# Kernel optimization log

Hardware: AMD Instinct MI355X
Metric: run time of the kernel (lower is better)

The kernel has to match this reference:

```python
import jax, jax.numpy as jnp
import numpy as np
from jax import lax

E = 5      # NUM_EXPERTS
K = 3      # top-k
DIN = 32 * 10 * 10  # 3200
DH = 128
NCLS = 10


def setup_inputs() -> dict:
    key = jax.random.key(0)
    ks = jax.random.split(key, 16)
    s = 0.02
    return {
        "x": jax.random.normal(ks[0], (8192, 1, 28, 28), dtype=jnp.float32),
        "conv1_w": jax.random.normal(ks[1], (16, 1, 5, 5), dtype=jnp.float32) * s,
        "conv1_b": jnp.zeros((16,), jnp.float32),
        "conv2_w": jax.random.normal(ks[2], (32, 16, 3, 3), dtype=jnp.float32) * s,
        "conv2_b": jnp.zeros((32,), jnp.float32),
        "Wg": jax.random.normal(ks[3], (DIN, E), dtype=jnp.float32) * s,
        "bg": jnp.zeros((E,), jnp.float32),
        "Wglu": jax.random.normal(ks[4], (DIN, E), dtype=jnp.float32) * s,
        "bglu": jnp.zeros((E,), jnp.float32),
        "W1e": jax.random.normal(ks[5], (E, DIN, DH), dtype=jnp.float32) * s,
        "b1e": jnp.zeros((E, DH), jnp.float32),
        "W2e": jax.random.normal(ks[6], (E, DH, DH), dtype=jnp.float32) * s,
        "b2e": jnp.zeros((E, DH), jnp.float32),
        "Ws": jax.random.normal(ks[7], (DH, NCLS), dtype=jnp.float32) * s,
        "bs": jnp.zeros((NCLS,), jnp.float32),
    }


def _conv(x, w, b):
    y = lax.conv_general_dilated(x, w, (1, 1), 'VALID',
                                 dimension_numbers=('NCHW', 'OIHW', 'NCHW'))
    return y + b[None, :, None, None]


def _maxpool2(x):
    return lax.reduce_window(x, -jnp.inf, lax.max, (1, 1, 2, 2), (1, 1, 2, 2), 'VALID')


def reference(x, conv1_w, conv1_b, conv2_w, conv2_b, Wg, bg, Wglu, bglu,
              W1e, b1e, W2e, b2e, Ws, bs):
    # conv feature extractor: [B,1,28,28] -> [B,3200]
    h = jax.nn.relu(_conv(x, conv1_w, conv1_b))          # [B,16,24,24]
    h = _maxpool2(h)                                     # [B,16,12,12]
    h = jax.nn.relu(_conv(h, conv2_w, conv2_b))          # [B,32,10,10]
    feat = h.reshape(h.shape[0], -1)                     # [B,3200]

    # GLU-gated router: logits * sigmoid(glu)
    h_act = feat @ Wg + bg                               # [B,E]
    h_glu_act = jax.nn.sigmoid(feat @ Wglu + bglu)       # [B,E]
    gate_logits = h_act * h_glu_act                      # [B,E]

    # top-K routing with softmax over selected logits
    top_v, top_i = lax.top_k(gate_logits, K)             # [B,K]
    top_w = jax.nn.softmax(top_v, axis=-1)               # [B,K]
    onehot = jax.nn.one_hot(top_i, E, dtype=feat.dtype)  # [B,K,E]
    weights = jnp.einsum('bk,bke->be', top_w, onehot)    # [B,E]

    # experts (dense compute of all E=5 experts, masked combine)
    e1 = jnp.tanh(jnp.einsum('bd,edh->beh', feat, W1e) + b1e[None])  # [B,E,128]
    e2 = jnp.tanh(jnp.einsum('beh,ehg->beg', e1, W2e) + b2e[None])   # [B,E,128]
    moe_out = jnp.einsum('beg,be->bg', e2, weights)      # [B,128]

    logits = moe_out @ Ws + bs                           # [B,10]
    return jax.nn.softmax(logits, axis=1)
```

## Files before the change

kernel.cpp:

```cpp
#include <hip/hip_runtime.h>
#include <stdint.h>

typedef unsigned short u16;
typedef __attribute__((ext_vector_type(8))) short bf16x8;
typedef __attribute__((ext_vector_type(4))) float f32x4;

#define MFMA16(a, b, c) __builtin_amdgcn_mfma_f32_16x16x32_bf16((a), (b), (c), 0, 0, 0)
#define GLD16(gp, lp) __builtin_amdgcn_global_load_lds( \
    (__attribute__((address_space(1))) void*)(gp), \
    (__attribute__((address_space(3))) void*)(lp), 16, 0, 0)

__device__ __forceinline__ u16 f2b(float f) {
  uint32_t u = __float_as_uint(f);
  u += 0x7FFFu + ((u >> 16) & 1u);
  return (u16)(u >> 16);
}
__device__ __forceinline__ float tanhfast(float x) {
  float e = __expf(2.f * x);
  return (e - 1.f) / (e + 1.f);
}


__global__ __launch_bounds__(256) void prep_misc_kernel(
    const float* __restrict__ c2w, const float* __restrict__ Wg,
    const float* __restrict__ Wglu, const float* __restrict__ W2e,
    u16* __restrict__ W2colF, u16* __restrict__ WcatT, u16* __restrict__ W2T) {
  int i = blockIdx.x * 256 + threadIdx.x;
  if (i < 5120) {
    int j = i & 7, l = (i >> 3) & 63, nt = (i >> 9) & 1, s = i >> 10;
    int k = s * 32 + ((l >> 4) & 3) * 8 + j;
    int n = (l & 15) + nt * 16;
    float v = 0.f;
    if (k < 144) {
      int kykx = k >> 4, ci = k & 15;
      int ky = kykx / 3, kx = kykx - ky * 3;
      v = c2w[((n * 16 + ci) * 3 + ky) * 3 + kx];
    }
    W2colF[i] = f2b(v);
  } else if (i < 56320) {
    int o = i - 5120;
    int s = o >> 9, rest = o & 511;
    int l = rest >> 3, j = rest & 7;
    int r = l & 15, c = (l >> 4) * 8 + j;
    int dref = c * 100 + s;
    float v = 0.f;
    if (r < 5) v = Wg[dref * 5 + r];
    else if (r < 10) v = Wglu[dref * 5 + (r - 5)];
    WcatT[o] = f2b(v);
  } else if (i < 138240) {
    int o = i - 56320;
    int e = o >> 14, rem = o & 16383;
    int g = rem >> 7, h = rem & 127;
    W2T[o] = f2b(W2e[(e * 128 + h) * 128 + g]);
  }
}

__global__ __launch_bounds__(256) void prep_w1t_kernel(
    const float* __restrict__ W1e, u16* __restrict__ W1T) {
  __shared__ u16 ts[64][128];
  int t = threadIdx.x;
  int e = blockIdx.x / 50, pt = blockIdx.x % 50;
  {
    int r64 = t >> 2;
    int ph = r64 >> 5, c = r64 & 31;
    int d = c * 100 + pt * 2 + ph;
    const float* src = W1e + ((size_t)e * 3200 + d) * 128 + (t & 3) * 32;
    u16* drow = &ts[r64][(t & 3) * 32];
#pragma unroll
    for (int u = 0; u < 8; u++) {
      float4 v = *(const float4*)(src + u * 4);
      drow[u * 4 + 0] = f2b(v.x); drow[u * 4 + 1] = f2b(v.y);
      drow[u * 4 + 2] = f2b(v.z); drow[u * 4 + 3] = f2b(v.w);
    }
  }
  __syncthreads();
#pragma unroll
  for (int k = 0; k < 4; k++) {
    int u = t + k * 256;
    int ph = u >> 9, nb = (u >> 6) & 7, l = u & 63;
    int lm = l & 15, lqf = l >> 4;
    u16 tmp[8];
#pragma unroll
    for (int j = 0; j < 8; j++)
      tmp[j] = ts[ph * 32 + lqf * 8 + j][nb * 16 + lm];
    *(uint4*)(W1T + (((size_t)((e * 100 + pt * 2 + ph) * 8 + nb)) << 9) + l * 8) =
        *(const uint4*)tmp;
  }
}

__global__ __launch_bounds__(192) void conv1_kernel(
    const float* __restrict__ x, const float* __restrict__ w1,
    const float* __restrict__ b1, u16* __restrict__ h1) {
  __shared__ float xs[784];
  __shared__ float wsh[400];
  __shared__ float bsh[16];
  int t = threadIdx.x, b = blockIdx.x;
  const float4* xg = (const float4*)(x + (size_t)b * 784);
  float4* xs4 = (float4*)xs;
  for (int i = t; i < 196; i += 192) xs4[i] = xg[i];
  for (int i = t; i < 400; i += 192) wsh[i] = w1[i];
  if (t < 16) bsh[t] = b1[t];
  __syncthreads();
  int oc = t & 15, q0 = t >> 4;
  float w[25];
#pragma unroll
  for (int k = 0; k < 25; k++) w[k] = wsh[oc * 25 + k];
  float bias = bsh[oc];
  u16* out = h1 + (size_t)b * 2304;
#pragma unroll
  for (int it = 0; it < 6; it++) {
    int q = q0 + 12 * it;
    int py = q / 6, px2 = q - py * 6;
    int y0 = 2 * py, x0 = 4 * px2;
    float win[6][8];
#pragma unroll
    for (int r = 0; r < 6; r++) {
      const float4* p = (const float4*)&xs[(y0 + r) * 28 + x0];
      float4 a = p[0], c = p[1];
      win[r][0] = a.x; win[r][1] = a.y; win[r][2] = a.z; win[r][3] = a.w;
      win[r][4] = c.x; win[r][5] = c.y; win[r][6] = c.z; win[r][7] = c.w;
    }
#pragma unroll
    for (int half = 0; half < 2; half++) {
      int dxb = 2 * half;
      float c00 = 0.f, c01 = 0.f, c10 = 0.f, c11 = 0.f;
#pragma unroll
      for (int ky = 0; ky < 5; ky++)
#pragma unroll
        for (int kx = 0; kx < 5; kx++) {
          float wv = w[ky * 5 + kx];
          c00 += wv * win[ky][dxb + kx];
          c01 += wv * win[ky][dxb + kx + 1];
          c10 += wv * win[ky + 1][dxb + kx];
          c11 += wv * win[ky + 1][dxb + kx + 1];
        }
      float m = fmaxf(fmaxf(c00, c01), fmaxf(c10, c11)) + bias;
      m = fmaxf(m, 0.f);
      int px = 2 * px2 + half;
      out[(py * 12 + px) * 16 + oc] = f2b(m);
    }
  }
}

__global__ __launch_bounds__(256) void conv2_kernel(
    const u16* __restrict__ h1, const u16* __restrict__ W2colF,
    const float* __restrict__ b2, u16* __restrict__ feat) {
  __shared__ u16 ct[4][16][32];
  int t = threadIdx.x;
  int w = t >> 6, l = t & 63;
  bf16x8 bfr[5][2];
#pragma unroll
  for (int s = 0; s < 5; s++)
#pragma unroll
    for (int nt = 0; nt < 2; nt++)
      bfr[s][nt] = *(const bf16x8*)(W2colF + ((size_t)(s * 2 + nt) * 64 + l) * 8);
  int lm = l & 15, lq = l >> 4, hi = l >> 5;
  int cib = (lq & 1) * 8;
  float bias0 = b2[lm], bias1 = b2[lm + 16];
  int g0 = blockIdx.x * 128 + w * 32;
#pragma unroll
  for (int sub = 0; sub < 2; sub++) {
    int g = g0 + sub * 16 + lm;
    uint32_t bimg = (uint32_t)(((uint64_t)(uint32_t)g * 1374389535ull) >> 37);
    int p = g - (int)bimg * 100;
    int y = (p * 205) >> 11;
    int xc = p - y * 10;
    const u16* base = h1 + (size_t)bimg * 2304;
    f32x4 acc0 = {0.f, 0.f, 0.f, 0.f}, acc1 = {0.f, 0.f, 0.f, 0.f};
#pragma unroll
    for (int s = 0; s < 5; s++) {
      int kk = 2 * s + hi;
      if (kk > 8) kk = 8;
      int ky = (kk * 11) >> 5;
      int kx = kk - ky * 3;
      int off = ((y + ky) * 12 + (xc + kx)) * 16 + cib;
      bf16x8 a = *(const bf16x8*)(base + off);
      acc0 = MFMA16(a, bfr[s][0], acc0);
      acc1 = MFMA16(a, bfr[s][1], acc1);
    }
#pragma unroll
    for (int rr = 0; rr < 4; rr++) {
      ct[w][lq * 4 + rr][lm]      = f2b(fmaxf(acc0[rr] + bias0, 0.f));
      ct[w][lq * 4 + rr][lm + 16] = f2b(fmaxf(acc1[rr] + bias1, 0.f));
    }
    int gg = g0 + sub * 16 + (l >> 2);
    uint32_t bi2 = (uint32_t)(((uint64_t)(uint32_t)gg * 1374389535ull) >> 37);
    int pp = gg - (int)bi2 * 100;
    int mt2 = (int)(bi2 >> 6), rb = (int)((bi2 >> 4) & 3), lmr = (int)(bi2 & 15);
    uint4 v = *(const uint4*)&ct[w][l >> 2][(l & 3) * 8];
    *(uint4*)(feat + (((size_t)(mt2 * 100 + pp) * 4 + rb) << 9) +
              ((l & 3) * 16 + lmr) * 8) = v;
  }
}

#define GEMM1_KLOOP(HASW, VMCSTR)                                              \
  {                                                                            \
    GLD16(pA, &lds[0][w * 512]);                                               \
    GLD16(pB1, &lds[0][2048 + w * 512]);                                       \
    GLD16(pB2, &lds[0][4096 + w * 512]);                                       \
    if (HASW) GLD16(pW, &lds[0][6144]);                                        \
    pA += 2048; pB1 += 4096; pB2 += 4096; pW += 512;                           \
    for (int s = 0; s < 100; s++) {                                            \
      int buf = s & 1;                                                         \
      if (s < 99) {                                                            \
        GLD16(pA, &lds[buf ^ 1][w * 512]);                                     \
        GLD16(pB1, &lds[buf ^ 1][2048 + w * 512]);                             \
        GLD16(pB2, &lds[buf ^ 1][4096 + w * 512]);                             \
        if (HASW) GLD16(pW, &lds[buf ^ 1][6144]);                              \
        pA += 2048; pB1 += 4096; pB2 += 4096; pW += 512;                       \
        asm volatile("s_waitcnt " VMCSTR ::: "memory");                        \
      } else {                                                                 \
        asm volatile("s_waitcnt vmcnt(0)" ::: "memory");                       \
      }                                                                        \
      asm volatile("s_barrier" ::: "memory");                                  \
      const u16* st = &lds[buf][0];                                            \
      bf16x8 af[2], bf[4];                                                     \
      _Pragma("unroll")                                                        \
      for (int i = 0; i < 2; i++)                                              \
        af[i] = *(const bf16x8*)(st + ((w & 1) * 2 + i) * 512 + l * 8);        \
      _Pragma("unroll")                                                        \
      for (int j = 0; j < 4; j++)                                              \
        bf[j] = *(const bf16x8*)(st + 2048 + ((w >> 1) * 4 + j) * 512 + l * 8);\
      _Pragma("unroll")                                                        \
      for (int i = 0; i < 2; i++)                                              \
        _Pragma("unroll")                                                      \
        for (int j = 0; j < 4; j++)                                            \
          acc[i][j] = MFMA16(af[i], bf[j], acc[i][j]);                         \
      if (HASW && w < 2) {                                                     \
        bf16x8 wf = *(const bf16x8*)(st + 6144 + l * 8);                       \
        racc[0] = MFMA16(af[0], wf, racc[0]);                                  \
        racc[1] = MFMA16(af[1], wf, racc[1]);                                  \
      }                                                                        \
      asm volatile("s_barrier" ::: "memory");                                  \
    }                                                                          \
  }

__global__ __launch_bounds__(256, 3) void gemm1_kernel(
    const u16* __restrict__ feat, const u16* __restrict__ W1T,
    const u16* __restrict__ WcatT, const float* __restrict__ b1e,
    const float* __restrict__ bg, const float* __restrict__ bglu,
    u16* __restrict__ e1b, float* __restrict__ rw) {
  __shared__ u16 lds[2][6656];
  int t = threadIdx.x, w = t >> 6, l = t & 63;
  int mt = blockIdx.x & 127;
  int e = blockIdx.x >> 7;
  size_t m0 = (size_t)mt * 64;
  int lm = l & 15, lq = l >> 4;
  int m_off = (w & 1) * 32, n_off = (w >> 1) * 64;

  const u16* pA = feat + (size_t)mt * 204800 + w * 512 + l * 8;
  const u16* pB1 = W1T + (size_t)e * 409600 + w * 512 + l * 8;
  const u16* pB2 = pB1 + 2048;
  const u16* pW = WcatT + l * 8;

  f32x4 acc[2][4] = {};
  f32x4 racc[2] = {};

  if (e == 0) GEMM1_KLOOP(true, "vmcnt(4)")
  else        GEMM1_KLOOP(false, "vmcnt(3)")

  float b1v[4];
#pragma unroll
  for (int j = 0; j < 4; j++) b1v[j] = b1e[e * 128 + n_off + 16 * j + lm];
  u16* E1t = &lds[0][0];
#pragma unroll
  for (int i = 0; i < 2; i++)
#pragma unroll
    for (int j = 0; j < 4; j++)
#pragma unroll
      for (int rr = 0; rr < 4; rr++) {
        int row = m_off + 16 * i + lq * 4 + rr;
        int col = n_off + 16 * j + lm;
        E1t[row * 128 + col] = f2b(tanhfast(acc[i][j][rr] + b1v[j]));
      }
  if (e == 0 && w < 2) {
    float* RACC = (float*)((char*)lds + 20480);
#pragma unroll
    for (int i = 0; i < 2; i++)
#pragma unroll
      for (int rr = 0; rr < 4; rr++)
        RACC[(m_off + 16 * i + lq * 4 + rr) * 16 + lm] = racc[i][rr];
  }
  __syncthreads();
#pragma unroll
  for (int k2 = 0; k2 < 4; k2++) {
    int u = t + k2 * 256;
    int row = u >> 4, sc = u & 15;
    uint4 v = *(const uint4*)(E1t + row * 128 + sc * 8);
    *(uint4*)(e1b + (m0 + row) * 640 + e * 128 + sc * 8) = v;
  }
  if (e == 0 && t < 64) {
    const float* RACC = (const float*)((char*)lds + 20480);
    float gt[5];
#pragma unroll
    for (int ee = 0; ee < 5; ee++) {
      float va = RACC[t * 16 + ee] + bg[ee];
      float vb = RACC[t * 16 + 5 + ee] + bglu[ee];
      gt[ee] = va * (1.f / (1.f + __expf(-vb)));
    }
    float w3[3]; int i3[3];
    unsigned used = 0;
#pragma unroll
    for (int k = 0; k < 3; k++) {
      float best = -1e30f; int bi = 0;
#pragma unroll
      for (int ee = 0; ee < 5; ee++)
        if (!((used >> ee) & 1u) && gt[ee] > best) { best = gt[ee]; bi = ee; }
      used |= 1u << bi; w3[k] = best; i3[k] = bi;
    }
    float s1 = __expf(w3[1] - w3[0]), s2 = __expf(w3[2] - w3[0]);
    float inv = 1.f / (1.f + s1 + s2);
    float o[5] = {0.f, 0.f, 0.f, 0.f, 0.f};
    o[i3[0]] = inv; o[i3[1]] = s1 * inv; o[i3[2]] = s2 * inv;
#pragma unroll
    for (int ee = 0; ee < 5; ee++) rw[(m0 + t) * 5 + ee] = o[ee];
  }
}

__global__ __launch_bounds__(256) void gemm2_head_kernel(
    const u16* __restrict__ e1b, const u16* __restrict__ W2T,
    const float* __restrict__ b2e, const float* __restrict__ rw,
    const float* __restrict__ Ws, const float* __restrict__ bs,
    float* __restrict__ out) {
  __shared__ u16 E1s[32][648];
  __shared__ float wssh[1280];
  __shared__ float rws[160];
  int t = threadIdx.x;
  int r0 = blockIdx.x * 32;
  {
    int row = t >> 3;
    const u16* src = e1b + (size_t)(r0 + row) * 640 + (t & 7) * 8;
    u16* drow = &E1s[row][(t & 7) * 8];
#pragma unroll
    for (int k = 0; k < 10; k++)
      *(uint4*)(drow + k * 64) = *(const uint4*)(src + k * 64);
  }
  if (t < 160) rws[t] = rw[r0 * 5 + t];
  for (int i = t; i < 1280; i += 256) wssh[i] = Ws[i];
  __syncthreads();

  int w = t >> 6, l = t & 63, lm = l & 15, lq = l >> 4;
  int mh = w & 1, nh = w >> 1;
  f32x4 moeacc[4] = {};
#pragma unroll
  for (int e = 0; e < 5; e++) {
    f32x4 acc[4] = {};
    const u16* w2e = W2T + e * 16384;
#pragma unroll
    for (int kk = 0; kk < 4; kk++) {
      bf16x8 a = *(const bf16x8*)&E1s[mh * 16 + lm][e * 128 + kk * 32 + lq * 8];
#pragma unroll
      for (int j = 0; j < 4; j++) {
        bf16x8 b = *(const bf16x8*)(w2e + (nh * 64 + 16 * j + lm) * 128 + kk * 32 + lq * 8);
        acc[j] = MFMA16(a, b, acc[j]);
      }
    }
#pragma unroll
    for (int j = 0; j < 4; j++) {
      float b2v = b2e[e * 128 + nh * 64 + 16 * j + lm];
#pragma unroll
      for (int rr = 0; rr < 4; rr++) {
        float v = tanhfast(acc[j][rr] + b2v);
        moeacc[j][rr] += rws[(mh * 16 + lq * 4 + rr) * 5 + e] * v;
      }
    }
  }
  __syncthreads();
  float* moes = (float*)&E1s[0][0];
#pragma unroll
  for (int j = 0; j < 4; j++)
#pragma unroll
    for (int rr = 0; rr < 4; rr++)
      moes[(mh * 16 + lq * 4 + rr) * 132 + nh * 64 + 16 * j + lm] = moeacc[j][rr];
  __syncthreads();
  float* parts = moes + 32 * 132;
  if (t < 128) {
    int row = t >> 2, qc = t & 3;
    float pl[10] = {};
    for (int cc = qc * 32; cc < qc * 32 + 32; cc++) {
      float mv = moes[row * 132 + cc];
#pragma unroll
      for (int cls = 0; cls < 10; cls++) pl[cls] += mv * wssh[cc * 10 + cls];
    }
#pragma unroll
    for (int cls = 0; cls < 10; cls++) parts[(row * 4 + qc) * 10 + cls] = pl[cls];
  }
  __syncthreads();
  if (t < 32) {
    float lg[10];
    float mx = -1e30f;
#pragma unroll
    for (int cls = 0; cls < 10; cls++) {
      lg[cls] = parts[(t * 4) * 10 + cls] + parts[(t * 4 + 1) * 10 + cls] +
                parts[(t * 4 + 2) * 10 + cls] + parts[(t * 4 + 3) * 10 + cls] + bs[cls];
      mx = fmaxf(mx, lg[cls]);
    }
    float sum = 0.f;
#pragma unroll
    for (int cls = 0; cls < 10; cls++) { lg[cls] = __expf(lg[cls] - mx); sum += lg[cls]; }
    float inv = 1.f / sum;
    float* orow = out + (size_t)(r0 + t) * 10;
#pragma unroll
    for (int cls = 0; cls < 10; cls++) orow[cls] = lg[cls] * inv;
  }
}

extern "C" void kernel_launch(void* const* d_in, const int* in_sizes, int n_in,
                              void* d_out, int out_size, void* d_ws, size_t ws_size,
                              hipStream_t stream) {
  const float* x    = (const float*)d_in[0];
  const float* c1w  = (const float*)d_in[1];
  const float* c1b  = (const float*)d_in[2];
  const float* c2w  = (const float*)d_in[3];
  const float* c2b  = (const float*)d_in[4];
  const float* Wg   = (const float*)d_in[5];
  const float* bg   = (const float*)d_in[6];
  const float* Wglu = (const float*)d_in[7];
  const float* bglu = (const float*)d_in[8];
  const float* W1e  = (const float*)d_in[9];
  const float* b1e  = (const float*)d_in[10];
  const float* W2e  = (const float*)d_in[11];
  const float* b2e  = (const float*)d_in[12];
  const float* Wsp  = (const float*)d_in[13];
  const float* bsp  = (const float*)d_in[14];
  char* ws = (char*)d_ws;
  u16* h1      = (u16*)(ws + 0);
  u16* e1b     = (u16*)(ws + 0);
  u16* feat    = (u16*)(ws + 37748736);
  u16* W1T     = (u16*)(ws + 90177536);
  u16* W2T     = (u16*)(ws + 94273536);
  u16* W2colF  = (u16*)(ws + 94437376);
  u16* WcatT   = (u16*)(ws + 94447616);
  float* rw    = (float*)(ws + 94550016);

  prep_misc_kernel<<<540, 256, 0, stream>>>(c2w, Wg, Wglu, W2e, W2colF, WcatT, W2T);
  prep_w1t_kernel<<<250, 256, 0, stream>>>(W1e, W1T);
  conv1_kernel<<<8192, 192, 0, stream>>>(x, c1w, c1b, h1);
  conv2_kernel<<<6400, 256, 0, stream>>>(h1, W2colF, c2b, feat);
  gemm1_kernel<<<640, 256, 0, stream>>>(feat, W1T, WcatT, b1e, bg, bglu, e1b, rw);
  gemm2_head_kernel<<<256, 256, 0, stream>>>(e1b, W2T, b2e, rw, Wsp, bsp,
                                             (float*)d_out);
}
```

Before: 244.7 us.

## Compute conv1 with bf16 MFMA implicit GEMM instead of scalar FMA

Rewrites conv1 to convert the input image to bf16 in shared memory and compute the 5x5 convolution as an implicit GEMM using two 16x16x32 bf16 MFMAs per tile. Conv outputs go to a shared buffer, and a second pass does the 2x2 maxpool, bias and ReLU. The block size changes from 192 to 256 threads. This replaces scalar fp32 FMA work with matrix cores, at the cost of rounding the input and the pre-pool activations to bf16 and a larger shared-memory footprint.

```diff
diff --git a/kernel.cpp b/kernel.cpp
--- a/kernel.cpp
+++ b/kernel.cpp
@@ -14,6 +14,9 @@
   uint32_t u = __float_as_uint(f);
   u += 0x7FFFu + ((u >> 16) & 1u);
   return (u16)(u >> 16);
+}
+__device__ __forceinline__ float b2f(u16 u) {
+  return __uint_as_float((uint32_t)u << 16);
 }
 __device__ __forceinline__ float tanhfast(float x) {
   float e = __expf(2.f * x);
@@ -88,57 +91,73 @@
   }
 }
 
-__global__ __launch_bounds__(192) void conv1_kernel(
+__global__ __launch_bounds__(256) void conv1_kernel(
     const float* __restrict__ x, const float* __restrict__ w1,
     const float* __restrict__ b1, u16* __restrict__ h1) {
-  __shared__ float xs[784];
+  __shared__ __align__(16) u16 img[928];
+  __shared__ __align__(16) u16 conv[11520];
   __shared__ float wsh[400];
   __shared__ float bsh[16];
-  int t = threadIdx.x, b = blockIdx.x;
+  int t = threadIdx.x, b = blockIdx.x, w = t >> 6, l = t & 63;
   const float4* xg = (const float4*)(x + (size_t)b * 784);
-  float4* xs4 = (float4*)xs;
-  for (int i = t; i < 196; i += 192) xs4[i] = xg[i];
-  for (int i = t; i < 400; i += 192) wsh[i] = w1[i];
+  if (t < 196) {
+    float4 v = xg[t];
+    uint2 p;
+    p.x = (uint32_t)f2b(v.x) | ((uint32_t)f2b(v.y) << 16);
+    p.y = (uint32_t)f2b(v.z) | ((uint32_t)f2b(v.w) << 16);
+    *(uint2*)&img[t * 4] = p;
+  } else if (t < 232) {
+    uint2 z = {0u, 0u};
+    *(uint2*)&img[784 + 4 * (t - 196)] = z;
+  }
+  for (int i = t; i < 400; i += 256) wsh[i] = w1[i];
   if (t < 16) bsh[t] = b1[t];
   __syncthreads();
-  int oc = t & 15, q0 = t >> 4;
-  float w[25];
-#pragma unroll
-  for (int k = 0; k < 25; k++) w[k] = wsh[oc * 25 + k];
-  float bias = bsh[oc];
-  u16* out = h1 + (size_t)b * 2304;
-#pragma unroll
-  for (int it = 0; it < 6; it++) {
-    int q = q0 + 12 * it;
-    int py = q / 6, px2 = q - py * 6;
-    int y0 = 2 * py, x0 = 4 * px2;
-    float win[6][8];
-#pragma unroll
-    for (int r = 0; r < 6; r++) {
-      const float4* p = (const float4*)&xs[(y0 + r) * 28 + x0];
-      float4 a = p[0], c = p[1];
-      win[r][0] = a.x; win[r][1] = a.y; win[r][2] = a.z; win[r][3] = a.w;
-      win[r][4] = c.x; win[r][5] = c.y; win[r][6] = c.z; win[r][7] = c.w;
-    }
-#pragma unroll
-    for (int half = 0; half < 2; half++) {
-      int dxb = 2 * half;
-      float c00 = 0.f, c01 = 0.f, c10 = 0.f, c11 = 0.f;
-#pragma unroll
-      for (int ky = 0; ky < 5; ky++)
-#pragma unroll
-        for (int kx = 0; kx < 5; kx++) {
-          float wv = w[ky * 5 + kx];
-          c00 += wv * win[ky][dxb + kx];
-          c01 += wv * win[ky][dxb + kx + 1];
-          c10 += wv * win[ky + 1][dxb + kx];
-          c11 += wv * win[ky + 1][dxb + kx + 1];
-        }
-      float m = fmaxf(fmaxf(c00, c01), fmaxf(c10, c11)) + bias;
-      m = fmaxf(m, 0.f);
-      int px = 2 * px2 + half;
-      out[(py * 12 + px) * 16 + oc] = f2b(m);
-    }
+
+  int lm = l & 15, q = l >> 4;
+  bf16x8 bw1 = {0, 0, 0, 0, 0, 0, 0, 0}, bw2 = {0, 0, 0, 0, 0, 0, 0, 0};
+#pragma unroll
+  for (int j = 0; j < 5; j++) {
+    bw1[j] = (short)f2b(wsh[lm * 25 + q * 5 + j]);
+    if (q == 0) bw2[j] = (short)f2b(wsh[lm * 25 + 20 + j]);
+  }
+
+#pragma unroll
+  for (int i = 0; i < 9; i++) {
+    int tt = w + i * 4;
+    int pos = tt * 16 + lm;
+    int y = (pos * 683) >> 14;
+    int xx = pos - y * 24;
+    int a1o = (y + q) * 28 + xx;
+    int a2o = a1o + 112;
+    bf16x8 a1, a2;
+#pragma unroll
+    for (int j = 0; j < 8; j++) {
+      a1[j] = (short)img[a1o + j];
+      a2[j] = (short)img[a2o + j];
+    }
+    f32x4 acc = {0.f, 0.f, 0.f, 0.f};
+    acc = MFMA16(a1, bw1, acc);
+    acc = MFMA16(a2, bw2, acc);
+    uint2 p;
+    p.x = (uint32_t)f2b(acc[0]) | ((uint32_t)f2b(acc[1]) << 16);
+    p.y = (uint32_t)f2b(acc[2]) | ((uint32_t)f2b(acc[3]) << 16);
+    *(uint2*)&conv[pos * 20 + q * 4] = p;
+  }
+  __syncthreads();
+
+  u16* hout = h1 + (size_t)b * 2304;
+#pragma unroll
+  for (int k2 = 0; k2 < 9; k2++) {
+    int u = t + k2 * 256;
+    int oc = u & 15, po = u >> 4;
+    int py = (po * 2731) >> 15;
+    int px = po - py * 12;
+    int cp = (py * 48 + px * 2) * 20 + oc;
+    float v0 = b2f(conv[cp]), v1 = b2f(conv[cp + 20]);
+    float v2 = b2f(conv[cp + 480]), v3 = b2f(conv[cp + 500]);
+    float m = fmaxf(fmaxf(v0, v1), fmaxf(v2, v3)) + bsh[oc];
+    hout[po * 16 + oc] = f2b(fmaxf(m, 0.f));
   }
 }
 
@@ -435,7 +454,7 @@
 
   prep_misc_kernel<<<540, 256, 0, stream>>>(c2w, Wg, Wglu, W2e, W2colF, WcatT, W2T);
   prep_w1t_kernel<<<250, 256, 0, stream>>>(W1e, W1T);
-  conv1_kernel<<<8192, 192, 0, stream>>>(x, c1w, c1b, h1);
+  conv1_kernel<<<8192, 256, 0, stream>>>(x, c1w, c1b, h1);
   conv2_kernel<<<6400, 256, 0, stream>>>(h1, W2colF, c2b, feat);
   gemm1_kernel<<<640, 256, 0, stream>>>(feat, W1T, WcatT, b1e, bg, bglu, e1b, rw);
   gemm2_head_kernel<<<256, 256, 0, stream>>>(e1b, W2T, b2e, rw, Wsp, bsp,
```

Result: slower. 270.1 us (+10.4%).
